# Optimization experiments

Hardware: AMD Instinct MI355X
Metric: run time of the kernel (lower is better)

Reference implementation:

```python
import jax, jax.numpy as jnp
import numpy as np
import math

B, T = 16, 60
N_CLASSES = 80
N_ANCHORS = 3
N_CH = 5 + N_CLASSES
STRIDES = (8, 16, 32)
IMG = 608
ANCHORS = np.array([[12,16],[19,36],[40,28],[36,75],[76,55],[72,146],[142,110],[192,243],[459,401]], dtype=np.float32)
IGNORE_THRE = 0.5


def _clip_log(x):
    # torch F.binary_cross_entropy clamps log at -100
    return jnp.maximum(jnp.log(x), -100.0)


def _bce_sum(p, t, w=None):
    l = -(t * _clip_log(p) + (1.0 - t) * _clip_log(1.0 - p))
    if w is not None:
        l = l * w
    return jnp.sum(l)


def _ciou_wh(wh_a, wh_b):
    # truth boxes are xyxy [0,0,w,h]; wh_a [B,T,2], wh_b [9,2] -> CIoU [B,T,9]
    wa = wh_a[..., 0:1]; ha = wh_a[..., 1:2]
    wb = wh_b[:, 0];     hb = wh_b[:, 1]
    iw = jnp.minimum(wa, wb); ih = jnp.minimum(ha, hb)
    en = ((iw > 0) & (ih > 0)).astype(wh_a.dtype)
    area_i = iw * ih * en
    area_u = wa * ha + wb * hb - area_i
    iou = area_i / area_u
    c2 = jnp.maximum(wa, wb) ** 2 + jnp.maximum(ha, hb) ** 2 + 1e-16
    rho2 = ((wa - wb) ** 2 + (ha - hb) ** 2) / 4.0
    v = (4.0 / math.pi ** 2) * (jnp.arctan(wa / ha) - jnp.arctan(wb / hb)) ** 2
    alpha = v / (1.0 - iou + v)
    return iou - (rho2 / c2 + v * alpha)


def _iou_xywh(pred, truth):
    # pred [B,N,4] (cx,cy,w,h), truth [B,T,4] -> IoU [B,N,T]
    p_xy = pred[:, :, None, :2]; p_wh = pred[:, :, None, 2:]
    t_xy = truth[:, None, :, :2]; t_wh = truth[:, None, :, 2:]
    tl = jnp.maximum(p_xy - p_wh * 0.5, t_xy - t_wh * 0.5)
    br = jnp.minimum(p_xy + p_wh * 0.5, t_xy + t_wh * 0.5)
    en = jnp.all(tl < br, axis=-1).astype(pred.dtype)
    area_i = jnp.prod(br - tl, axis=-1) * en
    area_p = pred[..., 2] * pred[..., 3]
    area_t = truth[..., 2] * truth[..., 3]
    return area_i / (area_p[:, :, None] + area_t[:, None, :] - area_i)


def _level_losses(x, labels, oid):
    dt = x.dtype
    stride = STRIDES[oid]
    fsize = IMG // stride
    Bsz = x.shape[0]
    out = x.reshape(Bsz, N_ANCHORS, N_CH, fsize, fsize).transpose(0, 1, 3, 4, 2)  # [B,A,F,F,C]
    sig = jax.nn.sigmoid(out)
    sxy, raw_wh, sobj, scls = sig[..., :2], out[..., 2:4], sig[..., 4], sig[..., 5:]

    all_anch = jnp.asarray(ANCHORS / stride, dt)           # [9,2] grid units
    masked_anch = all_anch[3 * oid: 3 * oid + 3]           # [3,2]
    g = jnp.arange(fsize, dtype=dt)
    px = sxy[..., 0] + g[None, None, None, :]
    py = sxy[..., 1] + g[None, None, :, None]
    pw = jnp.exp(raw_wh[..., 0]) * masked_anch[:, 0][None, :, None, None]
    ph = jnp.exp(raw_wh[..., 1]) * masked_anch[:, 1][None, :, None, None]
    pred = jnp.stack([px, py, pw, ph], axis=-1)            # [B,A,F,F,4]

    lab = jax.lax.stop_gradient(labels.astype(dt))         # targets carry no grad (as in torch)
    valid = jnp.sum(lab, axis=-1) > 0                      # [B,T]
    tx = (lab[..., 2] + lab[..., 0]) / (stride * 2.0)
    ty = (lab[..., 3] + lab[..., 1]) / (stride * 2.0)
    tw = (lab[..., 2] - lab[..., 0]) / stride
    th = (lab[..., 3] - lab[..., 1]) / stride
    ii = jnp.clip(tx.astype(jnp.int32), 0, fsize - 1)      # int16 trunc in torch, coords >= 0
    jj = jnp.clip(ty.astype(jnp.int32), 0, fsize - 1)

    ciou = _ciou_wh(jnp.stack([tw, th], -1), all_anch)     # [B,T,9]
    ciou = jnp.where(valid[..., None], ciou, -1e9)
    best_all = jnp.argmax(ciou, axis=-1)                   # [B,T]
    best_n = best_all % 3
    best_mask = (best_all // 3 == oid) & valid             # anchor owned by this level
    has_match = jnp.any(best_mask, axis=1)                 # [B]; torch `continue` if none

    truth_box = jnp.stack([tx, ty, tw, th], -1) * valid[..., None].astype(dt)
    ious = _iou_xywh(jax.lax.stop_gradient(pred).reshape(Bsz, -1, 4), truth_box)
    ious = jnp.where(valid[:, None, :], ious, 0.0)
    ignore = (jnp.max(ious, axis=-1) > IGNORE_THRE).reshape(Bsz, N_ANCHORS, fsize, fsize)
    obj_mask = jnp.where(has_match[:, None, None, None], 1.0 - ignore.astype(dt), jnp.asarray(1.0, dt))

    # scatter positive assignments; dummy batch row Bsz absorbs masked-out writes
    bidx = jnp.where(best_mask, jnp.arange(Bsz, dtype=jnp.int32)[:, None], Bsz)
    pad1 = lambda a: jnp.concatenate([a, jnp.zeros((1,) + a.shape[1:], a.dtype)], 0)
    obj_mask = pad1(obj_mask).at[bidx, best_n, jj, ii].set(1.0)[:Bsz]
    tgt_mask = jnp.zeros((Bsz + 1, N_ANCHORS, fsize, fsize, 4 + N_CLASSES), dt).at[bidx, best_n, jj, ii].set(1.0)[:Bsz]
    scale = jnp.sqrt(2.0 - tw * th / float(fsize * fsize))  # [B,T]
    tgt_scale = jnp.zeros((Bsz + 1, N_ANCHORS, fsize, fsize, 2), dt).at[bidx, best_n, jj, ii].set(
        jnp.broadcast_to(scale[..., None], scale.shape + (2,)))[:Bsz]
    aw = masked_anch[best_n, 0]; ah = masked_anch[best_n, 1]
    vec = jnp.concatenate([
        (tx - jnp.trunc(tx))[..., None],
        (ty - jnp.trunc(ty))[..., None],
        jnp.log(tw / aw + 1e-16)[..., None],
        jnp.log(th / ah + 1e-16)[..., None],
        jnp.ones_like(tx)[..., None],
        jax.nn.one_hot(lab[..., 4].astype(jnp.int32), N_CLASSES, dtype=dt),
    ], axis=-1)                                            # [B,T,N_CH]
    target = jnp.zeros((Bsz + 1, N_ANCHORS, fsize, fsize, N_CH), dt).at[bidx, best_n, jj, ii].set(vec)[:Bsz]

    o_xy = sxy * tgt_mask[..., :2]
    o_wh = raw_wh * tgt_mask[..., 2:4] * tgt_scale
    o_obj = sobj * obj_mask
    o_cls = scls * tgt_mask[..., 4:]
    t_xy = target[..., :2] * tgt_mask[..., :2]
    t_wh = target[..., 2:4] * tgt_mask[..., 2:4] * tgt_scale
    t_obj = target[..., 4] * obj_mask
    t_cls = target[..., 5:] * tgt_mask[..., 4:]

    l_xy = _bce_sum(o_xy, t_xy, tgt_scale * tgt_scale)
    l_wh = 0.5 * jnp.sum((o_wh - t_wh) ** 2)
    l_obj = _bce_sum(o_obj, t_obj)
    l_cls = _bce_sum(o_cls, t_cls)
    l_l2 = (jnp.sum((o_xy - t_xy) ** 2) + jnp.sum((o_wh - t_wh) ** 2)
            + jnp.sum((o_obj - t_obj) ** 2) + jnp.sum((o_cls - t_cls) ** 2))
    return l_xy, l_wh, l_obj, l_cls, l_l2


def setup_inputs() -> dict:
    key = jax.random.key(0)
    ks = jax.random.split(key, 8)
    x0 = jax.random.normal(ks[0], (B, N_ANCHORS * N_CH, 76, 76), jnp.float32)
    x1 = jax.random.normal(ks[1], (B, N_ANCHORS * N_CH, 38, 38), jnp.float32)
    x2 = jax.random.normal(ks[2], (B, N_ANCHORS * N_CH, 19, 19), jnp.float32)
    cx = jax.random.uniform(ks[3], (B, T), minval=70.0, maxval=538.0)
    cy = jax.random.uniform(ks[4], (B, T), minval=70.0, maxval=538.0)
    bw = jax.random.uniform(ks[5], (B, T), minval=8.0, maxval=128.0)
    bh = jax.random.uniform(ks[6], (B, T), minval=8.0, maxval=128.0)
    cls = jax.random.randint(ks[7], (B, T), 0, N_CLASSES).astype(jnp.float32)
    labels = jnp.stack([cx - bw / 2, cy - bh / 2, cx + bw / 2, cy + bh / 2, cls], axis=-1)
    nvalid = jax.random.randint(jax.random.fold_in(key, 99), (B,), 5, T + 1)
    mask = (jnp.arange(T)[None, :] < nvalid[:, None]).astype(jnp.float32)
    labels = labels * mask[..., None]  # zero padding rows (nlabel = rows with sum>0)
    return {"x0": x0, "x1": x1, "x2": x2, "labels": labels}


def reference(x0, x1, x2, labels):
    totals = [jnp.asarray(0.0, x0.dtype)] * 5
    for oid, x in enumerate((x0, x1, x2)):
        parts = _level_losses(x, labels, oid)
        totals = [a + b for a, b in zip(totals, parts)]
    l_xy, l_wh, l_obj, l_cls, l_l2 = totals
    loss = l_xy + l_wh + l_obj + l_cls
    return loss, l_xy, l_wh, l_obj, l_cls, l_l2
```

## Files before the change

kernel.cpp:

```cpp
#include <hip/hip_runtime.h>

#define BATCH 16
#define TT 60
#define NCLS 80
#define NB0 34
#define NB1 9
#define NB2 3
#define NBX (NB0 + NB1 + NB2)
#define NBLK (NBX * BATCH)

__constant__ float c_aw[9] = {12.f,19.f,40.f,36.f,76.f,72.f,142.f,192.f,459.f};
__constant__ float c_ah[9] = {16.f,36.f,28.f,75.f,55.f,146.f,110.f,243.f,401.f};

__device__ __forceinline__ float sigf(float x){ return 1.0f/(1.0f+expf(-x)); }
__device__ __forceinline__ float clogf_(float x){ return fmaxf(logf(x), -100.0f); }
__device__ __forceinline__ float bcef(float p, float t){
    return -(t*clogf_(p) + (1.0f-t)*clogf_(1.0f-p));
}

__global__ __launch_bounds__(256) void main_kernel(
    const float* __restrict__ x0, const float* __restrict__ x1,
    const float* __restrict__ x2, const float* __restrict__ labels,
    float* __restrict__ ws)
{
    const int bx = blockIdx.x, b = blockIdx.y, tid = threadIdx.x;
    int lvl, lb, fs;
    const float* x;
    if (bx < NB0)            { lvl = 0; lb = bx;             x = x0; fs = 76; }
    else if (bx < NB0 + NB1) { lvl = 1; lb = bx - NB0;       x = x1; fs = 38; }
    else                     { lvl = 2; lb = bx - NB0 - NB1; x = x2; fs = 19; }
    const float invs = 1.0f/(float)(8 << lvl);
    const int fs2 = fs*fs;
    const int ncell = 3*fs2;
    const int lin0 = lb*512 + tid;
    const int lin1 = lin0 + 256;

    __shared__ float  s_atan[9];
    __shared__ float4 s_box[TT];
    __shared__ int    s_mcell[TT], s_mcls[TT];
    __shared__ float  s_vx[TT], s_vy[TT], s_vw[TT], s_vh[TT], s_sc[TT];
    __shared__ int    s_nv, s_nm, s_qn;
    __shared__ int    s_qoff[TT], s_qcls[TT];

    float v0a=0,v1a=0,v2a=0,v3a=0,v4a=0, v0b=0,v1b=0,v2b=0,v3b=0,v4b=0;
    int a0=0,rem0=0,ci0=0,cj0=0, a1=0,rem1=0,ci1=0,cj1=0;
    if (lin0 < ncell) {
        a0 = lin0/fs2; rem0 = lin0 - a0*fs2; cj0 = rem0/fs; ci0 = rem0 - cj0*fs;
        const float* xb = x + ((size_t)b*255 + a0*85)*(size_t)fs2 + rem0;
        v0a = xb[0]; v1a = xb[(size_t)fs2]; v2a = xb[(size_t)2*fs2];
        v3a = xb[(size_t)3*fs2]; v4a = xb[(size_t)4*fs2];
    }
    if (lin1 < ncell) {
        a1 = lin1/fs2; rem1 = lin1 - a1*fs2; cj1 = rem1/fs; ci1 = rem1 - cj1*fs;
        const float* xb = x + ((size_t)b*255 + a1*85)*(size_t)fs2 + rem1;
        v0b = xb[0]; v1b = xb[(size_t)fs2]; v2b = xb[(size_t)2*fs2];
        v3b = xb[(size_t)3*fs2]; v4b = xb[(size_t)4*fs2];
    }
    float l0=0,l1=0,l2=0,l3=0,l4=0;
    if (tid < TT) {
        const float* lab = labels + ((size_t)b*TT + tid)*5;
        l0=lab[0]; l1=lab[1]; l2=lab[2]; l3=lab[3]; l4=lab[4];
    }
    if (tid < 9) s_atan[tid] = atanf(c_aw[tid]/c_ah[tid]);
    if (tid == 0) s_qn = 0;
    __syncthreads();

    if (tid < 64) {
        bool valid=false, best=false;
        float tx=0,ty=0,tw=0,th=0;
        int best_all=0;
        if (tid < TT) {
            valid = ((((l0+l1)+l2)+l3)+l4) > 0.0f;
            tx = (l2+l0)*(0.5f*invs);
            ty = (l3+l1)*(0.5f*invs);
            tw = (l2-l0)*invs;
            th = (l3-l1)*invs;
            if (valid) {
                float ta = atanf(tw/th);
                float twth = tw*th;
                float bestv = 0.0f;
                for (int k=0;k<9;k++){
                    float wb=c_aw[k]*invs, hb=c_ah[k]*invs;
                    float iw=fminf(tw,wb), ih=fminf(th,hb);
                    float en=(iw>0.f && ih>0.f)?1.f:0.f;
                    float ai=iw*ih*en;
                    float au=twth+wb*hb-ai;
                    float iou=ai/au;
                    float mw=fmaxf(tw,wb), mh=fmaxf(th,hb);
                    float c2=mw*mw+mh*mh+1e-16f;
                    float rho2=((tw-wb)*(tw-wb)+(th-hb)*(th-hb))*0.25f;
                    float da=ta-s_atan[k];
                    float v=0.40528473456935109f*da*da;
                    float alpha=v/((1.f-iou)+v);
                    float cv=iou-(rho2/c2+v*alpha);
                    if (k==0 || cv>bestv){ bestv=cv; best_all=k; }
                }
            }
        }
        int bn = best_all % 3;
        best = valid && ((best_all/3) == lvl);
        unsigned long long vm = __ballot(valid);
        unsigned long long bm = __ballot(best);
        unsigned long long below = (tid==0) ? 0ULL : ((1ULL<<tid)-1ULL);
        if (valid){
            int r = __popcll(vm & below);
            s_box[r] = make_float4(tx-0.5f*tw, ty-0.5f*th, tx+0.5f*tw, ty+0.5f*th);
        }
        if (best){
            int r = __popcll(bm & below);
            int ti=(int)tx, tj=(int)ty;
            int ii = ti<0?0:(ti>fs-1?fs-1:ti);
            int jj = tj<0?0:(tj>fs-1?fs-1:tj);
            s_mcell[r] = (bn*fs+jj)*fs+ii;
            s_mcls[r]  = (int)l4;
            s_sc[r]    = sqrtf(2.f - tw*th/(float)(fs*fs));
            s_vx[r]    = tx - truncf(tx);
            s_vy[r]    = ty - truncf(ty);
            float aw = c_aw[3*lvl+bn]*invs, ah = c_ah[3*lvl+bn]*invs;
            s_vw[r]    = logf(tw/aw + 1e-16f);
            s_vh[r]    = logf(th/ah + 1e-16f);
        }
        if (tid==0){ s_nv = __popcll(vm); s_nm = __popcll(bm); }
    }
    __syncthreads();

    const int nv = s_nv, nm = s_nm;
    float lxy=0.f, lwh=0.f, lobj=0.f, lcls=0.f, ll2=0.f;
    const bool c0 = (lin0 < ncell), c1 = (lin1 < ncell);
    if (c0 | c1) {
        const float sxa = sigf(v0a), sya = sigf(v1a), soa = sigf(v4a);
        const float sxb = sigf(v0b), syb = sigf(v1b), sob = sigf(v4b);
        const float awa = c_aw[3*lvl+a0]*invs, aha = c_ah[3*lvl+a0]*invs;
        const float awb = c_aw[3*lvl+a1]*invs, ahb = c_ah[3*lvl+a1]*invs;
        const float pxa = sxa + (float)ci0, pya = sya + (float)cj0;
        const float pxb = sxb + (float)ci1, pyb = syb + (float)cj1;
        const float pwa = expf(v2a)*awa, pha = expf(v3a)*aha;
        const float pwb = expf(v2b)*awb, phb = expf(v3b)*ahb;
        const float apa = pwa*pha, apb = pwb*phb;

        int mt0 = -1, mt1 = -1;
        for (int k=0;k<nm;k++){
            int mc = s_mcell[k];
            if (mc == lin0) mt0 = k;
            if (mc == lin1) mt1 = k;
        }

        bool iga = false, igb = false;
        if (nm > 0) {
            const float xla = pxa-0.5f*pwa, xra = pxa+0.5f*pwa;
            const float yla = pya-0.5f*pha, yra = pya+0.5f*pha;
            const float xlb = pxb-0.5f*pwb, xrb = pxb+0.5f*pwb;
            const float ylb = pyb-0.5f*phb, yrb = pyb+0.5f*phb;
            #pragma unroll 4
            for (int t=0;t<nv;t++){
                float4 tb = s_box[t];
                float at2 = (tb.z-tb.x)*(tb.w-tb.y);
                float wa = fminf(xra,tb.z) - fmaxf(xla,tb.x);
                float ha = fminf(yra,tb.w) - fmaxf(yla,tb.y);
                float wb = fminf(xrb,tb.z) - fmaxf(xlb,tb.x);
                float hb = fminf(yrb,tb.w) - fmaxf(ylb,tb.y);
                iga = iga || ((wa>0.f)&&(ha>0.f)&&(3.f*(wa*ha) > apa+at2));
                igb = igb || ((wb>0.f)&&(hb>0.f)&&(3.f*(wb*hb) > apb+at2));
            }
        }
        if (c0) {
            float om = (nm>0) ? (iga ? 0.f : 1.f) : 1.f;
            float t4 = 0.f;
            if (mt0 >= 0){ om = 1.f; t4 = 1.f; }
            float oo = soa*om, to = t4*om;
            lobj += bcef(oo, to);
            float d = oo - to; ll2 += d*d;
            if (mt0 >= 0) {
                float sc = s_sc[mt0], w2 = sc*sc;
                float mvx = s_vx[mt0], mvy = s_vy[mt0];
                lxy += w2*(bcef(sxa,mvx) + bcef(sya,mvy));
                float dx = sxa-mvx, dy = sya-mvy;
                float dw = sc*(v2a - s_vw[mt0]);
                float dh = sc*(v3a - s_vh[mt0]);
                lwh += 0.5f*(dw*dw + dh*dh);
                ll2 += dx*dx + dy*dy + dw*dw + dh*dh;
                int qi = atomicAdd(&s_qn, 1);
                s_qoff[qi] = (a0*85+5)*fs2 + rem0;
                s_qcls[qi] = s_mcls[mt0];
            }
        }
        if (c1) {
            float om = (nm>0) ? (igb ? 0.f : 1.f) : 1.f;
            float t4 = 0.f;
            if (mt1 >= 0){ om = 1.f; t4 = 1.f; }
            float oo = sob*om, to = t4*om;
            lobj += bcef(oo, to);
            float d = oo - to; ll2 += d*d;
            if (mt1 >= 0) {
                float sc = s_sc[mt1], w2 = sc*sc;
                float mvx = s_vx[mt1], mvy = s_vy[mt1];
                lxy += w2*(bcef(sxb,mvx) + bcef(syb,mvy));
                float dx = sxb-mvx, dy = syb-mvy;
                float dw = sc*(v2b - s_vw[mt1]);
                float dh = sc*(v3b - s_vh[mt1]);
                lwh += 0.5f*(dw*dw + dh*dh);
                ll2 += dx*dx + dy*dy + dw*dw + dh*dh;
                int qi = atomicAdd(&s_qn, 1);
                s_qoff[qi] = (a1*85+5)*fs2 + rem1;
                s_qcls[qi] = s_mcls[mt1];
            }
        }
    }
    __syncthreads();

    const int wid = tid>>6, ln = tid&63;
    const int qn = s_qn;
    for (int it = wid; it < qn; it += 4){
        const size_t base = (size_t)b*255*(size_t)fs2 + (size_t)s_qoff[it];
        const int cc = s_qcls[it];
        float p = sigf(x[base + (size_t)ln*fs2]);
        float tt = (ln==cc) ? 1.f : 0.f;
        lcls += bcef(p, tt);
        float dd = p - tt; ll2 += dd*dd;
        if (ln < NCLS-64) {
            int c = 64+ln;
            p = sigf(x[base + (size_t)c*fs2]);
            tt = (c==cc) ? 1.f : 0.f;
            lcls += bcef(p, tt);
            dd = p - tt; ll2 += dd*dd;
        }
    }

    for (int off=32; off>0; off>>=1){
        lxy  += __shfl_down(lxy,  off);
        lwh  += __shfl_down(lwh,  off);
        lobj += __shfl_down(lobj, off);
        lcls += __shfl_down(lcls, off);
        ll2  += __shfl_down(ll2,  off);
    }
    __shared__ float red[4][5];
    if (ln == 0){ red[wid][0]=lxy; red[wid][1]=lwh; red[wid][2]=lobj; red[wid][3]=lcls; red[wid][4]=ll2; }
    __syncthreads();
    if (tid == 0){
        const int blk = b*NBX + bx;
        ws[0*NBLK + blk] = red[0][0]+red[1][0]+red[2][0]+red[3][0];
        ws[1*NBLK + blk] = red[0][1]+red[1][1]+red[2][1]+red[3][1];
        ws[2*NBLK + blk] = red[0][2]+red[1][2]+red[2][2]+red[3][2];
        ws[3*NBLK + blk] = red[0][3]+red[1][3]+red[2][3]+red[3][3];
        ws[4*NBLK + blk] = red[0][4]+red[1][4]+red[2][4]+red[3][4];
    }
}

__global__ __launch_bounds__(256) void fin_kernel(const float* __restrict__ ws, float* __restrict__ out){
    const int tid = threadIdx.x;
    float s[5] = {0.f,0.f,0.f,0.f,0.f};
    for (int i = tid; i < NBLK; i += 256){
        #pragma unroll
        for (int c=0;c<5;c++) s[c] += ws[c*NBLK + i];
    }
    for (int off=32; off>0; off>>=1){
        #pragma unroll
        for (int c=0;c<5;c++) s[c] += __shfl_down(s[c], off);
    }
    __shared__ float red[4][5];
    const int wid = tid >> 6, ln = tid & 63;
    if (ln == 0){ for (int c=0;c<5;c++) red[wid][c] = s[c]; }
    __syncthreads();
    if (tid == 0){
        float t_xy  = red[0][0]+red[1][0]+red[2][0]+red[3][0];
        float t_wh  = red[0][1]+red[1][1]+red[2][1]+red[3][1];
        float t_obj = red[0][2]+red[1][2]+red[2][2]+red[3][2];
        float t_cls = red[0][3]+red[1][3]+red[2][3]+red[3][3];
        float t_l2  = red[0][4]+red[1][4]+red[2][4]+red[3][4];
        out[0] = t_xy + t_wh + t_obj + t_cls;
        out[1] = t_xy; out[2] = t_wh; out[3] = t_obj; out[4] = t_cls; out[5] = t_l2;
    }
}

extern "C" void kernel_launch(void* const* d_in, const int* in_sizes, int n_in,
                              void* d_out, int out_size, void* d_ws, size_t ws_size,
                              hipStream_t stream) {
    const float* x0 = (const float*)d_in[0];
    const float* x1 = (const float*)d_in[1];
    const float* x2 = (const float*)d_in[2];
    const float* labels = (const float*)d_in[3];
    float* out = (float*)d_out;
    float* ws = (float*)d_ws;

    main_kernel<<<dim3(NBX, BATCH), 256, 0, stream>>>(x0, x1, x2, labels, ws);
    fin_kernel<<<1, 256, 0, stream>>>(ws, out);
}
```

Baseline: 25.94 us.

## Replace shared-memory class-loss queue with per-wavefront ballot loop and drop barriers

Measured after the change: 23.99 us. -7.5%, faster.

```diff
diff --git a/kernel.cpp b/kernel.cpp
--- a/kernel.cpp
+++ b/kernel.cpp
@@ -39,8 +39,14 @@
     __shared__ float4 s_box[TT];
     __shared__ int    s_mcell[TT], s_mcls[TT];
     __shared__ float  s_vx[TT], s_vy[TT], s_vw[TT], s_vh[TT], s_sc[TT];
-    __shared__ int    s_nv, s_nm, s_qn;
-    __shared__ int    s_qoff[TT], s_qcls[TT];
+    __shared__ int    s_nv, s_nm;
+
+    float l0=0,l1=0,l2=0,l3=0,l4=0;
+    if (tid < TT) {
+        const float* lab = labels + ((size_t)b*TT + tid)*5;
+        l0=lab[0]; l1=lab[1]; l2=lab[2]; l3=lab[3]; l4=lab[4];
+    }
+    if (tid < 9) s_atan[tid] = atanf(c_aw[tid]/c_ah[tid]);
 
     float v0a=0,v1a=0,v2a=0,v3a=0,v4a=0, v0b=0,v1b=0,v2b=0,v3b=0,v4b=0;
     int a0=0,rem0=0,ci0=0,cj0=0, a1=0,rem1=0,ci1=0,cj1=0;
@@ -56,14 +62,6 @@
         v0b = xb[0]; v1b = xb[(size_t)fs2]; v2b = xb[(size_t)2*fs2];
         v3b = xb[(size_t)3*fs2]; v4b = xb[(size_t)4*fs2];
     }
-    float l0=0,l1=0,l2=0,l3=0,l4=0;
-    if (tid < TT) {
-        const float* lab = labels + ((size_t)b*TT + tid)*5;
-        l0=lab[0]; l1=lab[1]; l2=lab[2]; l3=lab[3]; l4=lab[4];
-    }
-    if (tid < 9) s_atan[tid] = atanf(c_aw[tid]/c_ah[tid]);
-    if (tid == 0) s_qn = 0;
-    __syncthreads();
 
     if (tid < 64) {
         bool valid=false, best=false;
@@ -126,7 +124,10 @@
 
     const int nv = s_nv, nm = s_nm;
     float lxy=0.f, lwh=0.f, lobj=0.f, lcls=0.f, ll2=0.f;
+    int mt0 = -1, mt1 = -1;
+    int qoff0 = 0, qoff1 = 0, cls0 = 0, cls1 = 0;
     const bool c0 = (lin0 < ncell), c1 = (lin1 < ncell);
+    float v2a_ = v2a, v3a_ = v3a, v2b_ = v2b, v3b_ = v3b;
     if (c0 | c1) {
         const float sxa = sigf(v0a), sya = sigf(v1a), soa = sigf(v4a);
         const float sxb = sigf(v0b), syb = sigf(v1b), sob = sigf(v4b);
@@ -134,11 +135,10 @@
         const float awb = c_aw[3*lvl+a1]*invs, ahb = c_ah[3*lvl+a1]*invs;
         const float pxa = sxa + (float)ci0, pya = sya + (float)cj0;
         const float pxb = sxb + (float)ci1, pyb = syb + (float)cj1;
-        const float pwa = expf(v2a)*awa, pha = expf(v3a)*aha;
-        const float pwb = expf(v2b)*awb, phb = expf(v3b)*ahb;
+        const float pwa = expf(v2a_)*awa, pha = expf(v3a_)*aha;
+        const float pwb = expf(v2b_)*awb, phb = expf(v3b_)*ahb;
         const float apa = pwa*pha, apb = pwb*phb;
 
-        int mt0 = -1, mt1 = -1;
         for (int k=0;k<nm;k++){
             int mc = s_mcell[k];
             if (mc == lin0) mt0 = k;
@@ -155,12 +155,12 @@
             for (int t=0;t<nv;t++){
                 float4 tb = s_box[t];
                 float at2 = (tb.z-tb.x)*(tb.w-tb.y);
-                float wa = fminf(xra,tb.z) - fmaxf(xla,tb.x);
-                float ha = fminf(yra,tb.w) - fmaxf(yla,tb.y);
-                float wb = fminf(xrb,tb.z) - fmaxf(xlb,tb.x);
-                float hb = fminf(yrb,tb.w) - fmaxf(ylb,tb.y);
-                iga = iga || ((wa>0.f)&&(ha>0.f)&&(3.f*(wa*ha) > apa+at2));
-                igb = igb || ((wb>0.f)&&(hb>0.f)&&(3.f*(wb*hb) > apb+at2));
+                float wa = fmaxf(fminf(xra,tb.z) - fmaxf(xla,tb.x), 0.f);
+                float ha = fmaxf(fminf(yra,tb.w) - fmaxf(yla,tb.y), 0.f);
+                float wb = fmaxf(fminf(xrb,tb.z) - fmaxf(xlb,tb.x), 0.f);
+                float hb = fmaxf(fminf(yrb,tb.w) - fmaxf(ylb,tb.y), 0.f);
+                iga = iga || (3.f*(wa*ha) > apa+at2);
+                igb = igb || (3.f*(wb*hb) > apb+at2);
             }
         }
         if (c0) {
@@ -175,13 +175,12 @@
                 float mvx = s_vx[mt0], mvy = s_vy[mt0];
                 lxy += w2*(bcef(sxa,mvx) + bcef(sya,mvy));
                 float dx = sxa-mvx, dy = sya-mvy;
-                float dw = sc*(v2a - s_vw[mt0]);
-                float dh = sc*(v3a - s_vh[mt0]);
+                float dw = sc*(v2a_ - s_vw[mt0]);
+                float dh = sc*(v3a_ - s_vh[mt0]);
                 lwh += 0.5f*(dw*dw + dh*dh);
                 ll2 += dx*dx + dy*dy + dw*dw + dh*dh;
-                int qi = atomicAdd(&s_qn, 1);
-                s_qoff[qi] = (a0*85+5)*fs2 + rem0;
-                s_qcls[qi] = s_mcls[mt0];
+                qoff0 = (a0*85+5)*fs2 + rem0;
+                cls0  = s_mcls[mt0];
             }
         }
         if (c1) {
@@ -196,23 +195,30 @@
                 float mvx = s_vx[mt1], mvy = s_vy[mt1];
                 lxy += w2*(bcef(sxb,mvx) + bcef(syb,mvy));
                 float dx = sxb-mvx, dy = syb-mvy;
-                float dw = sc*(v2b - s_vw[mt1]);
-                float dh = sc*(v3b - s_vh[mt1]);
+                float dw = sc*(v2b_ - s_vw[mt1]);
+                float dh = sc*(v3b_ - s_vh[mt1]);
                 lwh += 0.5f*(dw*dw + dh*dh);
                 ll2 += dx*dx + dy*dy + dw*dw + dh*dh;
-                int qi = atomicAdd(&s_qn, 1);
-                s_qoff[qi] = (a1*85+5)*fs2 + rem1;
-                s_qcls[qi] = s_mcls[mt1];
-            }
-        }
-    }
-    __syncthreads();
-
-    const int wid = tid>>6, ln = tid&63;
-    const int qn = s_qn;
-    for (int it = wid; it < qn; it += 4){
-        const size_t base = (size_t)b*255*(size_t)fs2 + (size_t)s_qoff[it];
-        const int cc = s_qcls[it];
+                qoff1 = (a1*85+5)*fs2 + rem1;
+                cls1  = s_mcls[mt1];
+            }
+        }
+    }
+
+    const int ln = tid & 63;
+    const size_t bbase = (size_t)b*255*(size_t)fs2;
+    unsigned long long mb0 = __ballot(mt0 >= 0);
+    unsigned long long mb1 = __ballot(mt1 >= 0);
+    while (mb0 | mb1) {
+        int src, qoff, cc;
+        if (mb0) {
+            src = __ffsll(mb0) - 1; mb0 &= mb0 - 1;
+            qoff = __shfl(qoff0, src); cc = __shfl(cls0, src);
+        } else {
+            src = __ffsll(mb1) - 1; mb1 &= mb1 - 1;
+            qoff = __shfl(qoff1, src); cc = __shfl(cls1, src);
+        }
+        const size_t base = bbase + (size_t)qoff;
         float p = sigf(x[base + (size_t)ln*fs2]);
         float tt = (ln==cc) ? 1.f : 0.f;
         lcls += bcef(p, tt);
@@ -234,6 +240,7 @@
         ll2  += __shfl_down(ll2,  off);
     }
     __shared__ float red[4][5];
+    const int wid = tid >> 6;
     if (ln == 0){ red[wid][0]=lxy; red[wid][1]=lwh; red[wid][2]=lobj; red[wid][3]=lcls; red[wid][4]=ll2; }
     __syncthreads();
     if (tid == 0){
```
